# Performance work log

Measured on AMD Instinct MI355X. Metric: run time of the kernel, lower is better.

Reference implementation:

```python
import jax, jax.numpy as jnp
import numpy as np

N = 50000      # nodes
E = 800000     # edges (avg degree 16)
C = 256        # channels
NOUT = 64      # n_out (hidden width of last conv's MLP)
NL = 4         # n_layers


def _glorot(key, shape):
    fan_in, fan_out = shape[-2], shape[-1]
    lim = np.sqrt(6.0 / (fan_in + fan_out)).astype(np.float32)
    return jax.random.uniform(key, shape, jnp.float32, -lim, lim)


def setup_inputs() -> dict:
    key = jax.random.key(0)
    ks = jax.random.split(key, 16)
    inp = {
        "x": jax.random.normal(ks[0], (N, C), jnp.float32),
        "src": jax.random.randint(ks[1], (E,), 0, N, jnp.int32),
        "dst": jax.random.randint(ks[2], (E,), 0, N, jnp.int32),
        # 3 inner GINConv MLPs: Dense(C,relu), Dense(C,relu), Dense(C,linear)
        "W1s": _glorot(ks[3], (NL - 1, C, C)),
        "b1s": jax.random.normal(ks[4], (NL - 1, C), jnp.float32) * 0.01,
        "W2s": _glorot(ks[5], (NL - 1, C, C)),
        "b2s": jax.random.normal(ks[6], (NL - 1, C), jnp.float32) * 0.01,
        "W3s": _glorot(ks[7], (NL - 1, C, C)),
        "b3s": jax.random.normal(ks[8], (NL - 1, C), jnp.float32) * 0.01,
        # final conv2 MLP: Dense(C,relu), Dense(NOUT,relu), Dense(C,linear)
        "cW1": _glorot(ks[9], (C, C)),
        "cb1": jax.random.normal(ks[10], (C,), jnp.float32) * 0.01,
        "cW2": _glorot(ks[11], (C, NOUT)),
        "cb2": jax.random.normal(ks[12], (NOUT,), jnp.float32) * 0.01,
        "cW3": _glorot(ks[13], (NOUT, C)),
        "cb3": jax.random.normal(ks[14], (C,), jnp.float32) * 0.01,
    }
    return inp


def reference(x, src, dst, W1s, b1s, W2s, b2s, W3s, b3s,
              cW1, cb1, cW2, cb2, cW3, cb3):
    def agg(h):
        # sparse A @ h: sum messages from src nodes into dst nodes
        return jax.ops.segment_sum(h[src], dst, num_segments=N)

    # inner GINConv layers (eps=0 -> (1+eps)*x == x)
    for l in range(NL - 1):
        h = x + agg(x)                       # [N, C]
        h = jax.nn.relu(h @ W1s[l] + b1s[l])
        h = jax.nn.relu(h @ W2s[l] + b2s[l])
        x = h @ W3s[l] + b3s[l]              # final Dense is linear

    # conv2: mlp_hidden=[C, NOUT] (relu) then final Dense(C, linear)
    h = x + agg(x)
    h = jax.nn.relu(h @ cW1 + cb1)
    h = jax.nn.relu(h @ cW2 + cb2)
    return h @ cW3 + cb3                     # [N, C]
```

## Files before the change

kernel.cpp:

```cpp
#include <hip/hip_runtime.h>

constexpr int C_DIM = 256;

using f32x4  = __attribute__((ext_vector_type(4))) float;
using bf16x8 = __attribute__((ext_vector_type(8))) short;


__global__ void k_zero_i32(int* __restrict__ p, int n) {
    int i = blockIdx.x * blockDim.x + threadIdx.x;
    if (i < n) p[i] = 0;
}

__global__ void k_hist(const int* __restrict__ dst, int E, int* __restrict__ cnt) {
    int e = blockIdx.x * blockDim.x + threadIdx.x;
    if (e < E) atomicAdd(&cnt[dst[e]], 1);
}

__global__ __launch_bounds__(1024) void k_scan(const int* __restrict__ cnt,
                                               int* __restrict__ off, int n) {
    __shared__ int sh[1024];
    const int tid = threadIdx.x;
    const int chunk = (n + 1023) >> 10;
    const int s = tid * chunk;
    const int e = min(s + chunk, n);
    int sum = 0;
    for (int i = s; i < e; i++) sum += cnt[i];
    sh[tid] = sum;
    __syncthreads();
    for (int ofs = 1; ofs < 1024; ofs <<= 1) {
        int t = (tid >= ofs) ? sh[tid - ofs] : 0;
        __syncthreads();
        sh[tid] += t;
        __syncthreads();
    }
    int run = sh[tid] - sum;
    for (int i = s; i < e; i++) { off[i] = run; run += cnt[i]; }
    if (tid == 1023) off[n] = sh[1023];
}

__global__ void k_copy_i32(const int* __restrict__ a, int* __restrict__ b, int n) {
    int i = blockIdx.x * blockDim.x + threadIdx.x;
    if (i < n) b[i] = a[i];
}

__global__ void k_scatter(const int* __restrict__ src, const int* __restrict__ dst, int E,
                          int* __restrict__ cur, int* __restrict__ adj) {
    int e = blockIdx.x * blockDim.x + threadIdx.x;
    if (e < E) {
        int p = atomicAdd(&cur[dst[e]], 1);
        adj[p] = src[e];
    }
}

__global__ __launch_bounds__(256) void k_agg(const float* __restrict__ x,
                                             const int* __restrict__ off,
                                             const int* __restrict__ adj,
                                             float* __restrict__ H, int n) {
    const int node = blockIdx.x * 4 + (threadIdx.x >> 6);
    if (node >= n) return;
    const int lane = threadIdx.x & 63;
    float4 acc = ((const float4*)(x + (size_t)node * C_DIM))[lane];
    const int s = off[node], e = off[node + 1];
    for (int j = s; j < e; j++) {
        const int sn = adj[j];
        float4 v = ((const float4*)(x + (size_t)sn * C_DIM))[lane];
        acc.x += v.x; acc.y += v.y; acc.z += v.z; acc.w += v.w;
    }
    ((float4*)(H + (size_t)node * C_DIM))[lane] = acc;
}

__global__ void k_split_w(const float* __restrict__ W, ushort* __restrict__ hi,
                          ushort* __restrict__ lo, int K, int M, int total) {
    int i = blockIdx.x * blockDim.x + threadIdx.x;
    if (i >= total) return;
    const int KM = K * M;
    const int mi = i / KM, rem = i - mi * KM;
    const int k = rem / M, m = rem - k * M;
    const float x = W[i];
    const uint u = __float_as_uint(x);
    const float hf = __uint_as_float(u & 0xffff0000u);
    const float lf = x - hf;
    const int oidx = mi * KM + m * K + k;
    hi[oidx] = (ushort)(u >> 16);
    lo[oidx] = (ushort)(__float_as_uint(lf) >> 16);
}

template <int RELU>
__global__ __launch_bounds__(256) void k_gemm_mfma(const float* __restrict__ X,
        const ushort* __restrict__ WtH, const ushort* __restrict__ WtL,
        const float* __restrict__ bias, float* __restrict__ Y,
        int n, int K, int M) {
    __shared__ ushort AsH[64][40], AsL[64][40], BsH[64][40], BsL[64][40];
    const int tid = threadIdx.x;
    const int l = tid & 63, w = tid >> 6;
    const int wr = w >> 1, wc = w & 1;
    const int lr = l & 15, lkq = l >> 4;
    const int lk = lkq * 8;
    const int row0 = blockIdx.x * 64, col0 = blockIdx.y * 64;
    f32x4 acc[2][2] = {};

    const int ar = tid >> 3, ac4 = tid & 7;
    const int bcol = tid >> 2, bq = tid & 3;

    for (int k0 = 0; k0 < K; k0 += 32) {
        __syncthreads();
#pragma unroll
        for (int h = 0; h < 2; h++) {
            const int r = ar + h * 32;
            const int row = row0 + r;
            float4 v = make_float4(0.f, 0.f, 0.f, 0.f);
            if (row < n) v = *(const float4*)(X + (size_t)row * K + k0 + ac4 * 4);
            const uint u0 = __float_as_uint(v.x), u1 = __float_as_uint(v.y);
            const uint u2 = __float_as_uint(v.z), u3 = __float_as_uint(v.w);
            uint2 hv;
            hv.x = (u0 >> 16) | (u1 & 0xffff0000u);
            hv.y = (u2 >> 16) | (u3 & 0xffff0000u);
            const float l0 = v.x - __uint_as_float(u0 & 0xffff0000u);
            const float l1 = v.y - __uint_as_float(u1 & 0xffff0000u);
            const float l2 = v.z - __uint_as_float(u2 & 0xffff0000u);
            const float l3 = v.w - __uint_as_float(u3 & 0xffff0000u);
            uint2 lv;
            lv.x = (__float_as_uint(l0) >> 16) | (__float_as_uint(l1) & 0xffff0000u);
            lv.y = (__float_as_uint(l2) >> 16) | (__float_as_uint(l3) & 0xffff0000u);
            *(uint2*)&AsH[r][ac4 * 4] = hv;
            *(uint2*)&AsL[r][ac4 * 4] = lv;
        }
        {
            const size_t g = (size_t)(col0 + bcol) * K + k0 + bq * 8;
            *(uint4*)&BsH[bcol][bq * 8] = *(const uint4*)(WtH + g);
            *(uint4*)&BsL[bcol][bq * 8] = *(const uint4*)(WtL + g);
        }
        __syncthreads();

        bf16x8 aH[2], aL[2], bH[2], bL[2];
#pragma unroll
        for (int f = 0; f < 2; f++) {
            aH[f] = *(const bf16x8*)&AsH[wr * 32 + f * 16 + lr][lk];
            aL[f] = *(const bf16x8*)&AsL[wr * 32 + f * 16 + lr][lk];
            bH[f] = *(const bf16x8*)&BsH[wc * 32 + f * 16 + lr][lk];
            bL[f] = *(const bf16x8*)&BsL[wc * 32 + f * 16 + lr][lk];
        }
#pragma unroll
        for (int fi = 0; fi < 2; fi++)
#pragma unroll
            for (int fj = 0; fj < 2; fj++) {
                acc[fi][fj] = __builtin_amdgcn_mfma_f32_16x16x32_bf16(aH[fi], bH[fj], acc[fi][fj], 0, 0, 0);
                acc[fi][fj] = __builtin_amdgcn_mfma_f32_16x16x32_bf16(aL[fi], bH[fj], acc[fi][fj], 0, 0, 0);
                acc[fi][fj] = __builtin_amdgcn_mfma_f32_16x16x32_bf16(aH[fi], bL[fj], acc[fi][fj], 0, 0, 0);
            }
    }

#pragma unroll
    for (int fi = 0; fi < 2; fi++)
#pragma unroll
        for (int fj = 0; fj < 2; fj++) {
            const int col = col0 + wc * 32 + fj * 16 + lr;
            const float bv = bias[col];
#pragma unroll
            for (int r = 0; r < 4; r++) {
                const int row = row0 + wr * 32 + fi * 16 + lkq * 4 + r;
                if (row < n) {
                    float v = acc[fi][fj][r] + bv;
                    if (RELU) v = fmaxf(v, 0.f);
                    Y[(size_t)row * M + col] = v;
                }
            }
        }
}


extern "C" void kernel_launch(void* const* d_in, const int* in_sizes, int n_in,
                              void* d_out, int out_size, void* d_ws, size_t ws_size,
                              hipStream_t stream) {
    const float* x   = (const float*)d_in[0];
    const int*   src = (const int*)d_in[1];
    const int*   dst = (const int*)d_in[2];
    const float* W1s = (const float*)d_in[3];
    const float* b1s = (const float*)d_in[4];
    const float* W2s = (const float*)d_in[5];
    const float* b2s = (const float*)d_in[6];
    const float* W3s = (const float*)d_in[7];
    const float* b3s = (const float*)d_in[8];
    const float* cW1 = (const float*)d_in[9];
    const float* cb1 = (const float*)d_in[10];
    const float* cW2 = (const float*)d_in[11];
    const float* cb2 = (const float*)d_in[12];
    const float* cW3 = (const float*)d_in[13];
    const float* cb3 = (const float*)d_in[14];

    const int n  = in_sizes[0] / C_DIM;
    const int E  = in_sizes[1];
    const int NL = in_sizes[3] / (C_DIM * C_DIM);

    char* w = (char*)d_ws;
    size_t o = 0;
    auto take = [&](size_t bytes) -> char* {
        char* p = w + o;
        o = (o + bytes + 255) & ~(size_t)255;
        return p;
    };
    int*   off  = (int*)take(sizeof(int) * (size_t)(n + 1));
    int*   cur  = (int*)take(sizeof(int) * (size_t)n);
    int*   adj  = (int*)take(sizeof(int) * (size_t)E);
    float* bufH = (float*)take(sizeof(float) * (size_t)n * C_DIM);
    float* bufA = (float*)take(sizeof(float) * (size_t)n * C_DIM);
    const int szW  = NL * C_DIM * C_DIM;
    const int szC1 = C_DIM * C_DIM;
    const int szC2 = C_DIM * 64;
    const int szC3 = 64 * C_DIM;
    ushort* W1tH = (ushort*)take(2ull * szW);
    ushort* W1tL = (ushort*)take(2ull * szW);
    ushort* W2tH = (ushort*)take(2ull * szW);
    ushort* W2tL = (ushort*)take(2ull * szW);
    ushort* W3tH = (ushort*)take(2ull * szW);
    ushort* W3tL = (ushort*)take(2ull * szW);
    ushort* C1tH = (ushort*)take(2ull * szC1);
    ushort* C1tL = (ushort*)take(2ull * szC1);
    ushort* C2tH = (ushort*)take(2ull * szC2);
    ushort* C2tL = (ushort*)take(2ull * szC2);
    ushort* C3tH = (ushort*)take(2ull * szC3);
    ushort* C3tL = (ushort*)take(2ull * szC3);
    float* out = (float*)d_out;

    const dim3 b256(256);

    k_split_w<<<dim3((szW + 255) / 256), b256, 0, stream>>>(W1s, W1tH, W1tL, C_DIM, C_DIM, szW);
    k_split_w<<<dim3((szW + 255) / 256), b256, 0, stream>>>(W2s, W2tH, W2tL, C_DIM, C_DIM, szW);
    k_split_w<<<dim3((szW + 255) / 256), b256, 0, stream>>>(W3s, W3tH, W3tL, C_DIM, C_DIM, szW);
    k_split_w<<<dim3((szC1 + 255) / 256), b256, 0, stream>>>(cW1, C1tH, C1tL, C_DIM, C_DIM, szC1);
    k_split_w<<<dim3((szC2 + 255) / 256), b256, 0, stream>>>(cW2, C2tH, C2tL, C_DIM, 64, szC2);
    k_split_w<<<dim3((szC3 + 255) / 256), b256, 0, stream>>>(cW3, C3tH, C3tL, 64, C_DIM, szC3);

    k_zero_i32<<<dim3((n + 255) / 256), b256, 0, stream>>>(cur, n);
    k_hist<<<dim3((E + 255) / 256), b256, 0, stream>>>(dst, E, cur);
    k_scan<<<1, 1024, 0, stream>>>(cur, off, n);
    k_copy_i32<<<dim3((n + 255) / 256), b256, 0, stream>>>(off, cur, n);
    k_scatter<<<dim3((E + 255) / 256), b256, 0, stream>>>(src, dst, E, cur, adj);

    const int gx = (n + 63) / 64;
    const dim3 gAgg((n + 3) / 4);

    const float* xp = x;
    for (int l = 0; l < NL; l++) {
        const size_t wo = (size_t)l * C_DIM * C_DIM;
        k_agg<<<gAgg, b256, 0, stream>>>(xp, off, adj, bufH, n);
        k_gemm_mfma<1><<<dim3(gx, 4), b256, 0, stream>>>(bufH, W1tH + wo, W1tL + wo, b1s + l * C_DIM, bufA, n, C_DIM, C_DIM);
        k_gemm_mfma<1><<<dim3(gx, 4), b256, 0, stream>>>(bufA, W2tH + wo, W2tL + wo, b2s + l * C_DIM, out,  n, C_DIM, C_DIM);
        k_gemm_mfma<0><<<dim3(gx, 4), b256, 0, stream>>>(out,  W3tH + wo, W3tL + wo, b3s + l * C_DIM, bufA, n, C_DIM, C_DIM);
        xp = bufA;
    }
    k_agg<<<gAgg, b256, 0, stream>>>(xp, off, adj, bufH, n);
    k_gemm_mfma<1><<<dim3(gx, 4), b256, 0, stream>>>(bufH, C1tH, C1tL, cb1, bufA, n, C_DIM, C_DIM);
    k_gemm_mfma<1><<<dim3(gx, 1), b256, 0, stream>>>(bufA, C2tH, C2tL, cb2, bufH, n, C_DIM, 64);
    k_gemm_mfma<0><<<dim3(gx, 4), b256, 0, stream>>>(bufH, C3tH, C3tL, cb3, out, n, 64, C_DIM);
}
```

Baseline: 1.248 ms.

## Store activations as pre-split bf16 hi/lo planes and enlarge GEMM row tile

Intermediate activations are now kept as separate bf16 high and low planes. The aggregation kernel and the GEMM epilogues produce these planes directly, so the GEMMs load the split operands straight into shared memory and no longer split fp32 values into hi/lo inside the main loop. The GEMM row tile grows from 64 to 128 rows, which halves how often each weight tile is reloaded. The output buffer is reused as scratch for one plane pair. In exchange, the gather in aggregation now reads two 8-byte-per-lane streams per neighbour instead of one 16-byte stream, and the larger tile uses more registers and shared memory.

```diff
diff --git a/kernel.cpp b/kernel.cpp
--- a/kernel.cpp
+++ b/kernel.cpp
@@ -4,6 +4,9 @@
 
 using f32x4  = __attribute__((ext_vector_type(4))) float;
 using bf16x8 = __attribute__((ext_vector_type(8))) short;
+
+__device__ __forceinline__ float uf(uint u) { return __uint_as_float(u); }
+__device__ __forceinline__ uint  fu(float f) { return __float_as_uint(f); }
 
 
 __global__ void k_zero_i32(int* __restrict__ p, int n) {
@@ -52,21 +55,53 @@
     }
 }
 
-__global__ __launch_bounds__(256) void k_agg(const float* __restrict__ x,
-                                             const int* __restrict__ off,
-                                             const int* __restrict__ adj,
-                                             float* __restrict__ H, int n) {
+template <int SPLIT_IN>
+__global__ __launch_bounds__(256) void k_agg2(const float* __restrict__ xf,
+        const ushort* __restrict__ xh, const ushort* __restrict__ xl,
+        const int* __restrict__ off, const int* __restrict__ adj,
+        ushort* __restrict__ Hh, ushort* __restrict__ Hl, int n) {
     const int node = blockIdx.x * 4 + (threadIdx.x >> 6);
     if (node >= n) return;
     const int lane = threadIdx.x & 63;
-    float4 acc = ((const float4*)(x + (size_t)node * C_DIM))[lane];
+    float a0, a1, a2, a3;
+    if (SPLIT_IN) {
+        const uint2 h  = ((const uint2*)(xh + (size_t)node * C_DIM))[lane];
+        const uint2 lo = ((const uint2*)(xl + (size_t)node * C_DIM))[lane];
+        a0 = uf(h.x << 16) + uf(lo.x << 16);
+        a1 = uf(h.x & 0xffff0000u) + uf(lo.x & 0xffff0000u);
+        a2 = uf(h.y << 16) + uf(lo.y << 16);
+        a3 = uf(h.y & 0xffff0000u) + uf(lo.y & 0xffff0000u);
+    } else {
+        const float4 v = ((const float4*)(xf + (size_t)node * C_DIM))[lane];
+        a0 = v.x; a1 = v.y; a2 = v.z; a3 = v.w;
+    }
     const int s = off[node], e = off[node + 1];
     for (int j = s; j < e; j++) {
         const int sn = adj[j];
-        float4 v = ((const float4*)(x + (size_t)sn * C_DIM))[lane];
-        acc.x += v.x; acc.y += v.y; acc.z += v.z; acc.w += v.w;
-    }
-    ((float4*)(H + (size_t)node * C_DIM))[lane] = acc;
+        if (SPLIT_IN) {
+            const uint2 h  = ((const uint2*)(xh + (size_t)sn * C_DIM))[lane];
+            const uint2 lo = ((const uint2*)(xl + (size_t)sn * C_DIM))[lane];
+            a0 += uf(h.x << 16) + uf(lo.x << 16);
+            a1 += uf(h.x & 0xffff0000u) + uf(lo.x & 0xffff0000u);
+            a2 += uf(h.y << 16) + uf(lo.y << 16);
+            a3 += uf(h.y & 0xffff0000u) + uf(lo.y & 0xffff0000u);
+        } else {
+            const float4 v = ((const float4*)(xf + (size_t)sn * C_DIM))[lane];
+            a0 += v.x; a1 += v.y; a2 += v.z; a3 += v.w;
+        }
+    }
+    const uint u0 = fu(a0), u1 = fu(a1), u2 = fu(a2), u3 = fu(a3);
+    uint2 ho, lo_;
+    ho.x = (u0 >> 16) | (u1 & 0xffff0000u);
+    ho.y = (u2 >> 16) | (u3 & 0xffff0000u);
+    const float r0 = a0 - uf(u0 & 0xffff0000u);
+    const float r1 = a1 - uf(u1 & 0xffff0000u);
+    const float r2 = a2 - uf(u2 & 0xffff0000u);
+    const float r3 = a3 - uf(u3 & 0xffff0000u);
+    lo_.x = (fu(r0) >> 16) | (fu(r1) & 0xffff0000u);
+    lo_.y = (fu(r2) >> 16) | (fu(r3) & 0xffff0000u);
+    ((uint2*)(Hh + (size_t)node * C_DIM))[lane] = ho;
+    ((uint2*)(Hl + (size_t)node * C_DIM))[lane] = lo_;
 }
 
 __global__ void k_split_w(const float* __restrict__ W, ushort* __restrict__ hi,
@@ -77,71 +112,62 @@
     const int mi = i / KM, rem = i - mi * KM;
     const int k = rem / M, m = rem - k * M;
     const float x = W[i];
-    const uint u = __float_as_uint(x);
-    const float hf = __uint_as_float(u & 0xffff0000u);
-    const float lf = x - hf;
+    const uint u = fu(x);
+    const float lf = x - uf(u & 0xffff0000u);
     const int oidx = mi * KM + m * K + k;
     hi[oidx] = (ushort)(u >> 16);
-    lo[oidx] = (ushort)(__float_as_uint(lf) >> 16);
-}
-
-template <int RELU>
-__global__ __launch_bounds__(256) void k_gemm_mfma(const float* __restrict__ X,
-        const ushort* __restrict__ WtH, const ushort* __restrict__ WtL,
-        const float* __restrict__ bias, float* __restrict__ Y,
+    lo[oidx] = (ushort)(fu(lf) >> 16);
+}
+
+template <int RELU, int OSPLIT>
+__global__ __launch_bounds__(256) void k_gemm3(const ushort* __restrict__ Ah,
+        const ushort* __restrict__ Al, const ushort* __restrict__ Bh,
+        const ushort* __restrict__ Bl, const float* __restrict__ bias,
+        float* __restrict__ Yf, ushort* __restrict__ Yh, ushort* __restrict__ Yl,
         int n, int K, int M) {
-    __shared__ ushort AsH[64][40], AsL[64][40], BsH[64][40], BsL[64][40];
+    __shared__ ushort AsH[128][40], AsL[128][40], BsH[64][40], BsL[64][40];
     const int tid = threadIdx.x;
     const int l = tid & 63, w = tid >> 6;
     const int wr = w >> 1, wc = w & 1;
-    const int lr = l & 15, lkq = l >> 4;
-    const int lk = lkq * 8;
-    const int row0 = blockIdx.x * 64, col0 = blockIdx.y * 64;
-    f32x4 acc[2][2] = {};
-
-    const int ar = tid >> 3, ac4 = tid & 7;
-    const int bcol = tid >> 2, bq = tid & 3;
+    const int lr = l & 15, lkq = l >> 4, lk = lkq * 8;
+    const int row0 = blockIdx.x * 128, col0 = blockIdx.y * 64;
+    f32x4 acc[4][2] = {};
+
+    const int sr = tid >> 1, sh = (tid & 1) * 16;
+    const int bc = tid >> 2, bq = (tid & 3) * 8;
 
     for (int k0 = 0; k0 < K; k0 += 32) {
         __syncthreads();
-#pragma unroll
-        for (int h = 0; h < 2; h++) {
-            const int r = ar + h * 32;
-            const int row = row0 + r;
-            float4 v = make_float4(0.f, 0.f, 0.f, 0.f);
-            if (row < n) v = *(const float4*)(X + (size_t)row * K + k0 + ac4 * 4);
-            const uint u0 = __float_as_uint(v.x), u1 = __float_as_uint(v.y);
-            const uint u2 = __float_as_uint(v.z), u3 = __float_as_uint(v.w);
-            uint2 hv;
-            hv.x = (u0 >> 16) | (u1 & 0xffff0000u);
-            hv.y = (u2 >> 16) | (u3 & 0xffff0000u);
-            const float l0 = v.x - __uint_as_float(u0 & 0xffff0000u);
-            const float l1 = v.y - __uint_as_float(u1 & 0xffff0000u);
-            const float l2 = v.z - __uint_as_float(u2 & 0xffff0000u);
-            const float l3 = v.w - __uint_as_float(u3 & 0xffff0000u);
-            uint2 lv;
-            lv.x = (__float_as_uint(l0) >> 16) | (__float_as_uint(l1) & 0xffff0000u);
-            lv.y = (__float_as_uint(l2) >> 16) | (__float_as_uint(l3) & 0xffff0000u);
-            *(uint2*)&AsH[r][ac4 * 4] = hv;
-            *(uint2*)&AsL[r][ac4 * 4] = lv;
-        }
-        {
-            const size_t g = (size_t)(col0 + bcol) * K + k0 + bq * 8;
-            *(uint4*)&BsH[bcol][bq * 8] = *(const uint4*)(WtH + g);
-            *(uint4*)&BsL[bcol][bq * 8] = *(const uint4*)(WtL + g);
-        }
+        const int arow = row0 + sr;
+        if (arow < n) {
+            const size_t ga = (size_t)arow * K + k0 + sh;
+            *(uint4*)&AsH[sr][sh]     = *(const uint4*)(Ah + ga);
+            *(uint4*)&AsH[sr][sh + 8] = *(const uint4*)(Ah + ga + 8);
+            *(uint4*)&AsL[sr][sh]     = *(const uint4*)(Al + ga);
+            *(uint4*)&AsL[sr][sh + 8] = *(const uint4*)(Al + ga + 8);
+        } else {
+            const uint4 z = make_uint4(0, 0, 0, 0);
+            *(uint4*)&AsH[sr][sh] = z; *(uint4*)&AsH[sr][sh + 8] = z;
+            *(uint4*)&AsL[sr][sh] = z; *(uint4*)&AsL[sr][sh + 8] = z;
+        }
+        const size_t gb = (size_t)(col0 + bc) * K + k0 + bq;
+        *(uint4*)&BsH[bc][bq] = *(const uint4*)(Bh + gb);
+        *(uint4*)&BsL[bc][bq] = *(const uint4*)(Bl + gb);
         __syncthreads();
 
-        bf16x8 aH[2], aL[2], bH[2], bL[2];
+        bf16x8 aH[4], aL[4], bH[2], bL[2];
+#pragma unroll
+        for (int f = 0; f < 4; f++) {
+            aH[f] = *(const bf16x8*)&AsH[wr * 64 + f * 16 + lr][lk];
+            aL[f] = *(const bf16x8*)&AsL[wr * 64 + f * 16 + lr][lk];
+        }
 #pragma unroll
         for (int f = 0; f < 2; f++) {
-            aH[f] = *(const bf16x8*)&AsH[wr * 32 + f * 16 + lr][lk];
-            aL[f] = *(const bf16x8*)&AsL[wr * 32 + f * 16 + lr][lk];
             bH[f] = *(const bf16x8*)&BsH[wc * 32 + f * 16 + lr][lk];
             bL[f] = *(const bf16x8*)&BsL[wc * 32 + f * 16 + lr][lk];
         }
 #pragma unroll
-        for (int fi = 0; fi < 2; fi++)
+        for (int fi = 0; fi < 4; fi++)
 #pragma unroll
             for (int fj = 0; fj < 2; fj++) {
                 acc[fi][fj] = __builtin_amdgcn_mfma_f32_16x16x32_bf16(aH[fi], bH[fj], acc[fi][fj], 0, 0, 0);
@@ -151,18 +177,26 @@
     }
 
 #pragma unroll
-    for (int fi = 0; fi < 2; fi++)
+    for (int fi = 0; fi < 4; fi++)
 #pragma unroll
         for (int fj = 0; fj < 2; fj++) {
             const int col = col0 + wc * 32 + fj * 16 + lr;
             const float bv = bias[col];
 #pragma unroll
             for (int r = 0; r < 4; r++) {
-                const int row = row0 + wr * 32 + fi * 16 + lkq * 4 + r;
+                const int row = row0 + wr * 64 + fi * 16 + lkq * 4 + r;
                 if (row < n) {
                     float v = acc[fi][fj][r] + bv;
                     if (RELU) v = fmaxf(v, 0.f);
-                    Y[(size_t)row * M + col] = v;
+                    const size_t oi = (size_t)row * M + col;
+                    if (OSPLIT) {
+                        const uint u = fu(v);
+                        const float rv = v - uf(u & 0xffff0000u);
+                        Yh[oi] = (ushort)(u >> 16);
+                        Yl[oi] = (ushort)(fu(rv) >> 16);
+                    } else {
+                        Yf[oi] = v;
+                    }
                 }
             }
         }
@@ -192,18 +226,24 @@
     const int E  = in_sizes[1];
     const int NL = in_sizes[3] / (C_DIM * C_DIM);
 
-    char* w = (char*)d_ws;
+    char* wsp = (char*)d_ws;
     size_t o = 0;
     auto take = [&](size_t bytes) -> char* {
-        char* p = w + o;
+        char* p = wsp + o;
         o = (o + bytes + 255) & ~(size_t)255;
         return p;
     };
-    int*   off  = (int*)take(sizeof(int) * (size_t)(n + 1));
-    int*   cur  = (int*)take(sizeof(int) * (size_t)n);
-    int*   adj  = (int*)take(sizeof(int) * (size_t)E);
-    float* bufH = (float*)take(sizeof(float) * (size_t)n * C_DIM);
-    float* bufA = (float*)take(sizeof(float) * (size_t)n * C_DIM);
+    int* off = (int*)take(sizeof(int) * (size_t)(n + 1));
+    int* cur = (int*)take(sizeof(int) * (size_t)n);
+    int* adj = (int*)take(sizeof(int) * (size_t)E);
+    const size_t plane = (size_t)n * C_DIM;
+    ushort* B0h = (ushort*)take(2 * plane);
+    ushort* B0l = (ushort*)take(2 * plane);
+    ushort* B1h = (ushort*)take(2 * plane);
+    ushort* B1l = (ushort*)take(2 * plane);
+    ushort* B2h = (ushort*)d_out;
+    ushort* B2l = B2h + plane;
+
     const int szW  = NL * C_DIM * C_DIM;
     const int szC1 = C_DIM * C_DIM;
     const int szC2 = C_DIM * 64;
@@ -237,20 +277,28 @@
     k_copy_i32<<<dim3((n + 255) / 256), b256, 0, stream>>>(off, cur, n);
     k_scatter<<<dim3((E + 255) / 256), b256, 0, stream>>>(src, dst, E, cur, adj);
 
-    const int gx = (n + 63) / 64;
+    const int gx = (n + 127) / 128;
     const dim3 gAgg((n + 3) / 4);
 
-    const float* xp = x;
-    for (int l = 0; l < NL; l++) {
-        const size_t wo = (size_t)l * C_DIM * C_DIM;
-        k_agg<<<gAgg, b256, 0, stream>>>(xp, off, adj, bufH, n);
-        k_gemm_mfma<1><<<dim3(gx, 4), b256, 0, stream>>>(bufH, W1tH + wo, W1tL + wo, b1s + l * C_DIM, bufA, n, C_DIM, C_DIM);
-        k_gemm_mfma<1><<<dim3(gx, 4), b256, 0, stream>>>(bufA, W2tH + wo, W2tL + wo, b2s + l * C_DIM, out,  n, C_DIM, C_DIM);
-        k_gemm_mfma<0><<<dim3(gx, 4), b256, 0, stream>>>(out,  W3tH + wo, W3tL + wo, b3s + l * C_DIM, bufA, n, C_DIM, C_DIM);
-        xp = bufA;
-    }
-    k_agg<<<gAgg, b256, 0, stream>>>(xp, off, adj, bufH, n);
-    k_gemm_mfma<1><<<dim3(gx, 4), b256, 0, stream>>>(bufH, C1tH, C1tL, cb1, bufA, n, C_DIM, C_DIM);
-    k_gemm_mfma<1><<<dim3(gx, 1), b256, 0, stream>>>(bufA, C2tH, C2tL, cb2, bufH, n, C_DIM, 64);
-    k_gemm_mfma<0><<<dim3(gx, 4), b256, 0, stream>>>(bufH, C3tH, C3tL, cb3, out, n, 64, C_DIM);
-}
+    for (int lyr = 0; lyr < NL; lyr++) {
+        const size_t wo = (size_t)lyr * C_DIM * C_DIM;
+        if (lyr == 0)
+            k_agg2<0><<<gAgg, b256, 0, stream>>>(x, nullptr, nullptr, off, adj, B1h, B1l, n);
+        else
+            k_agg2<1><<<gAgg, b256, 0, stream>>>(nullptr, B0h, B0l, off, adj, B1h, B1l, n);
+        k_gemm3<1, 1><<<dim3(gx, 4), b256, 0, stream>>>(B1h, B1l, W1tH + wo, W1tL + wo,
+            b1s + lyr * C_DIM, nullptr, B2h, B2l, n, C_DIM, C_DIM);
+        k_gemm3<1, 1><<<dim3(gx, 4), b256, 0, stream>>>(B2h, B2l, W2tH + wo, W2tL + wo,
+            b2s + lyr * C_DIM, nullptr, B1h, B1l, n, C_DIM, C_DIM);
+        k_gemm3<0, 1><<<dim3(gx, 4), b256, 0, stream>>>(B1h, B1l, W3tH + wo, W3tL + wo,
+            b3s + lyr * C_DIM, nullptr, B0h, B0l, n, C_DIM, C_DIM);
+    }
+
+    k_agg2<1><<<gAgg, b256, 0, stream>>>(nullptr, B0h, B0l, off, adj, B1h, B1l, n);
+    k_gemm3<1, 1><<<dim3(gx, 4), b256, 0, stream>>>(B1h, B1l, C1tH, C1tL, cb1,
+        nullptr, B2h, B2l, n, C_DIM, C_DIM);
+    k_gemm3<1, 1><<<dim3(gx, 1), b256, 0, stream>>>(B2h, B2l, C2tH, C2tL, cb2,
+        nullptr, B1h, B1l, n, C_DIM, 64);
+    k_gemm3<0, 0><<<dim3(gx, 4), b256, 0, stream>>>(B1h, B1l, C3tH, C3tL, cb3,
+        out, nullptr, nullptr, n, 64, C_DIM);
+}
```

Measured after the change: 1.460 ms. 1.17x slower.
